# Performance work log

Hardware: AMD Instinct MI355X
Metric: run time of the kernel (lower is better)

The kernel has to match this reference:

```python
import jax, jax.numpy as jnp
import numpy as np

INPUT_DIM = 512
N_TREES = 64
TREE_DEPTH = 3
N_LEAVES = 2 ** TREE_DEPTH      # 8
N_INTERNAL = 2 ** TREE_DEPTH - 1  # 7
PPT = N_INTERNAL * (INPUT_DIM + 1) + N_LEAVES * 2  # params per tree = 3607
BATCH = 65536


def setup_inputs() -> dict:
    key = jax.random.key(0)
    k1, k2, k3 = jax.random.split(key, 3)
    x = jax.random.normal(k1, (BATCH, INPUT_DIM), dtype=jnp.float32)
    tree_params = jax.random.normal(k2, (1, N_TREES * PPT), dtype=jnp.float32)
    tree_weights = jax.random.normal(k3, (1, N_TREES), dtype=jnp.float32)
    return {"x": x, "tree_params": tree_params, "tree_weights": tree_weights}


def reference(x, tree_params, tree_weights):
    # Unpack all trees at once: [T, ppt]
    p = tree_params[0].reshape(N_TREES, PPT)
    split_w = p[:, : N_INTERNAL * INPUT_DIM].reshape(N_TREES, N_INTERNAL, INPUT_DIM)
    split_b = p[:, N_INTERNAL * INPUT_DIM : N_INTERNAL * (INPUT_DIM + 1)]  # [T, I]
    leaf_logits = p[:, N_INTERNAL * (INPUT_DIM + 1) :].reshape(N_TREES, N_LEAVES, 2)

    # decisions: [B, T, I]
    decisions = jax.nn.sigmoid(jnp.einsum('bd,tid->bti', x, split_w) + split_b[None])

    # Replicate the original indexing quirk: leaf_probs column j (a tree NODE index)
    # gets factor d_i if j == 2i+1 (and j < n_leaves), (1-d_i) if j == 2i+2.
    # Column 0 remains 1.0; each other column gets exactly one factor.
    cols = []
    for j in range(N_LEAVES):
        if j == 0:
            cols.append(jnp.ones_like(decisions[:, :, 0]))
        elif j % 2 == 1:
            i = (j - 1) // 2
            cols.append(decisions[:, :, i] if i < N_INTERNAL else jnp.ones_like(decisions[:, :, 0]))
        else:
            i = (j - 2) // 2
            cols.append(1.0 - decisions[:, :, i] if i < N_INTERNAL else jnp.ones_like(decisions[:, :, 0]))
    leaf_probs = jnp.stack(cols, axis=-1)  # [B, T, L]
    leaf_probs = leaf_probs / (leaf_probs.sum(axis=-1, keepdims=True) + 1e-8)

    leaf_dist = jax.nn.softmax(leaf_logits, axis=-1)  # [T, L, 2]
    tree_out = jnp.einsum('btl,tlc->btc', leaf_probs, leaf_dist)  # [B, T, 2]
    return jnp.einsum('btc,t->bc', tree_out, tree_weights[0])  # [B, 2]
```

## Files before the change

kernel.cpp:

```cpp
#include <hip/hip_runtime.h>
#include <stdint.h>


#define KDIM 512
#define PPT 3607

typedef _Float16 f16x8 __attribute__((ext_vector_type(8)));
typedef float f32x4 __attribute__((ext_vector_type(4)));


__global__ __launch_bounds__(128) void prep_kernel(const float* __restrict__ p,
                                                   const float* __restrict__ tw,
                                                   _Float16* __restrict__ Wh,
                                                   float* __restrict__ biasN,
                                                   float* __restrict__ AB) {
    const int c = blockIdx.x;
    const int t = c >> 2, i = c & 3;
    const float* wsrc = p + t * PPT + i * KDIM;
    for (int k = threadIdx.x; k < KDIM; k += 128)
        Wh[c * KDIM + k] = (_Float16)wsrc[k];
    if (threadIdx.x == 0)
        biasN[c] = p[t * PPT + 7 * KDIM + i];
    if (threadIdx.x == 64 && c < 64) {
        const int tt = c;
        const float* lg = p + tt * PPT + 7 * 513;
        const float w = tw[tt];
        float ld[8][2];
#pragma unroll
        for (int j = 0; j < 8; ++j) {
            float a = lg[2 * j], b = lg[2 * j + 1];
            float m = fmaxf(a, b);
            float e0 = expf(a - m), e1 = expf(b - m);
            float s = e0 + e1;
            ld[j][0] = e0 / s; ld[j][1] = e1 / s;
        }
        float* o = AB + tt * 10;
#pragma unroll
        for (int cc = 0; cc < 2; ++cc) {
            o[0 + cc] = w * (ld[0][cc] + ld[2][cc] + ld[4][cc] + ld[6][cc]);
            o[2 + cc] = w * (ld[1][cc] - ld[2][cc]);
            o[4 + cc] = w * (ld[3][cc] - ld[4][cc]);
            o[6 + cc] = w * (ld[5][cc] - ld[6][cc]);
            o[8 + cc] = w * (ld[7][cc]);
        }
    }
}

#define XBUF_STRIDE 8192
#define W_BASE 16384
#define WBUF_STRIDE 16384
#define EPI_STRIDE 260
#define AB_OFF 66560
#define PART_OFF 69120
#define LDS_BYTES 73216

__device__ __forceinline__ void gll16(const void* g, void* l) {
    __builtin_amdgcn_global_load_lds((const __attribute__((address_space(1))) uint32_t*)g,
                                     (__attribute__((address_space(3))) uint32_t*)l, 16, 0, 0);
}

__device__ __forceinline__ f16x8 cvt8(float4 a, float4 b) {
    f16x8 h;
    h[0] = (_Float16)a.x; h[1] = (_Float16)a.y; h[2] = (_Float16)a.z; h[3] = (_Float16)a.w;
    h[4] = (_Float16)b.x; h[5] = (_Float16)b.y; h[6] = (_Float16)b.z; h[7] = (_Float16)b.w;
    return h;
}

__global__ __launch_bounds__(512, 4) void main_kernel(const float* __restrict__ X,
                                                      const _Float16* __restrict__ Wh,
                                                      const float* __restrict__ biasN,
                                                      const float* __restrict__ ABg,
                                                      float* __restrict__ out) {
    extern __shared__ char smem[];
    const int tid = threadIdx.x;
    const int lane = tid & 63;
    const int w = tid >> 6;
    const int wm = w >> 2;
    const int wn = w & 3;
    const int gr0 = blockIdx.x * 128;

    {
        float* abl = (float*)(smem + AB_OFF);
        for (int i = tid; i < 640; i += 512) abl[i] = ABg[i];
    }
    asm volatile("s_waitcnt vmcnt(0)" ::: "memory");

    const float* Xrow = X + (size_t)(gr0 + (tid >> 2)) * KDIM + (tid & 3) * 8;
    const int wOffX = ((tid >> 2) << 6) + ((((tid & 3) ^ ((tid >> 3) & 3))) << 4);

    const _Float16* srcW[2];
    int dW[2];
#pragma unroll
    for (int i = 0; i < 2; ++i) {
        int colW = i * 128 + w * 16 + (lane >> 2);
        int kW = ((lane & 3) << 3) ^ (((colW >> 1) & 3) << 3);
        srcW[i] = Wh + (size_t)colW * KDIM + kW;
        dW[i] = (i * 512 + w * 64 + lane) * 16;
    }

    const int kb = (lane >> 4) << 3;
    const int kws = kb ^ (((lane >> 1) & 3) << 3);
    const int bColBase = (wn * 64 + (lane & 15)) * 32;
    const int aOff = ((lane & 15) << 6)
                   + (((lane >> 4) ^ (((lane & 15) >> 1) & 3)) << 4);

    f32x4 acc[4][4];
#pragma unroll
    for (int rt = 0; rt < 4; ++rt)
#pragma unroll
        for (int nt = 0; nt < 4; ++nt)
            acc[rt][nt] = (f32x4){0.f, 0.f, 0.f, 0.f};

    float4 xr[2][2];

    {
        float4 x0a = *(const float4*)(Xrow + 0);
        float4 x0b = *(const float4*)(Xrow + 4);
        gll16(srcW[0] + 0 * 32, smem + W_BASE + 0 * WBUF_STRIDE + dW[0]);
        gll16(srcW[1] + 0 * 32, smem + W_BASE + 0 * WBUF_STRIDE + dW[1]);
        xr[1][0] = *(const float4*)(Xrow + 1 * 32);
        xr[1][1] = *(const float4*)(Xrow + 1 * 32 + 4);
        gll16(srcW[0] + 1 * 32, smem + W_BASE + 1 * WBUF_STRIDE + dW[0]);
        gll16(srcW[1] + 1 * 32, smem + W_BASE + 1 * WBUF_STRIDE + dW[1]);
        *(f16x8*)(smem + 0 * XBUF_STRIDE + wOffX) = cvt8(x0a, x0b);
    }

#pragma unroll 16
    for (int kt = 0; kt < 16; ++kt) {
        if (kt <= 13) {
            xr[kt & 1][0] = *(const float4*)(Xrow + (kt + 2) * 32);
            xr[kt & 1][1] = *(const float4*)(Xrow + (kt + 2) * 32 + 4);
        }
        if (kt <= 13)      asm volatile("s_waitcnt vmcnt(4)" ::: "memory");
        else if (kt == 14) asm volatile("s_waitcnt vmcnt(2)" ::: "memory");
        else               asm volatile("s_waitcnt vmcnt(0)" ::: "memory");
        __builtin_amdgcn_s_barrier();
        if (kt <= 13) {
            char* wb = smem + W_BASE + ((kt + 2) % 3) * WBUF_STRIDE;
            gll16(srcW[0] + (kt + 2) * 32, wb + dW[0]);
            gll16(srcW[1] + (kt + 2) * 32, wb + dW[1]);
        }
        if (kt <= 14)
            *(f16x8*)(smem + ((kt + 1) & 1) * XBUF_STRIDE + wOffX) =
                cvt8(xr[(kt + 1) & 1][0], xr[(kt + 1) & 1][1]);
        {
            const _Float16* Wl = (const _Float16*)(smem + W_BASE + (kt % 3) * WBUF_STRIDE);
            const char* Xl = smem + (kt & 1) * XBUF_STRIDE + wm * 4096;
            f16x8 bfr[4];
#pragma unroll
            for (int nt = 0; nt < 4; ++nt)
                bfr[nt] = *(const f16x8*)&Wl[bColBase + nt * 512 + kws];
#pragma unroll
            for (int rt = 0; rt < 4; ++rt) {
                f16x8 af = *(const f16x8*)(Xl + rt * 1024 + aOff);
#pragma unroll
                for (int nt = 0; nt < 4; ++nt)
                    acc[rt][nt] = __builtin_amdgcn_mfma_f32_16x16x32_f16(af, bfr[nt], acc[rt][nt], 0, 0, 0);
            }
        }
    }

    __syncthreads();

    for (int p = 0; p < 2; ++p) {
        if (wm == p) {
            float bl[4];
#pragma unroll
            for (int nt = 0; nt < 4; ++nt) bl[nt] = biasN[wn * 64 + nt * 16 + (lane & 15)];
            float* ep = (float*)smem;
#pragma unroll
            for (int rt = 0; rt < 4; ++rt)
#pragma unroll
                for (int nt = 0; nt < 4; ++nt) {
                    const int col = wn * 64 + nt * 16 + (lane & 15);
#pragma unroll
                    for (int reg = 0; reg < 4; ++reg) {
                        const int rowl = rt * 16 + ((lane >> 4) << 2) + reg;
                        float z = acc[rt][nt][reg] + bl[nt];
                        ep[rowl * EPI_STRIDE + col] = __builtin_amdgcn_rcpf(1.f + __expf(-z));
                    }
                }
        }
        __syncthreads();
        {
            const float* ep = (const float*)smem;
            const float* abl = (const float*)(smem + AB_OFF);
            float* pb = (float*)(smem + PART_OFF);
            const int r = lane;
            float s0 = 0.f, s1 = 0.f;
#pragma unroll
            for (int j = 0; j < 8; ++j) {
                const int t = w * 8 + j;
                float4 dv = *(const float4*)&ep[r * EPI_STRIDE + t * 4];
                const float* abt = &abl[t * 10];
                float inv = __builtin_amdgcn_rcpf(4.f + dv.w + 1e-8f);
                s0 += (abt[0] + dv.x * abt[2] + dv.y * abt[4] + dv.z * abt[6] + dv.w * abt[8]) * inv;
                s1 += (abt[1] + dv.x * abt[3] + dv.y * abt[5] + dv.z * abt[7] + dv.w * abt[9]) * inv;
            }
            pb[(w * 64 + r) * 2 + 0] = s0;
            pb[(w * 64 + r) * 2 + 1] = s1;
        }
        __syncthreads();
        if (tid < 128) {
            const float* pb = (const float*)(smem + PART_OFF);
            const int r = tid >> 1, c = tid & 1;
            float s = 0.f;
#pragma unroll
            for (int g = 0; g < 8; ++g) s += pb[(g * 64 + r) * 2 + c];
            out[(size_t)(gr0 + p * 64 + r) * 2 + c] = s;
        }
        if (p == 0) __syncthreads();
    }
}

extern "C" void kernel_launch(void* const* d_in, const int* in_sizes, int n_in,
                              void* d_out, int out_size, void* d_ws, size_t ws_size,
                              hipStream_t stream) {
    const float* x  = (const float*)d_in[0];
    const float* tp = (const float*)d_in[1];
    const float* tw = (const float*)d_in[2];
    float* out = (float*)d_out;

    _Float16* Wh = (_Float16*)d_ws;
    float* biasN = (float*)((char*)d_ws + 262144);
    float* AB    = (float*)((char*)d_ws + 263168);

    (void)hipFuncSetAttribute((const void*)reinterpret_cast<const void*>(&main_kernel),
                              hipFuncAttributeMaxDynamicSharedMemorySize, LDS_BYTES);

    prep_kernel<<<256, 128, 0, stream>>>(tp, tw, Wh, biasN, AB);
    main_kernel<<<512, 512, LDS_BYTES, stream>>>(x, Wh, biasN, AB, out);
}
```

Baseline: 42.37 us.

## Switch W staging to double buffering with nontemporal X loads

The main GEMM loop now keeps two LDS buffers for the f16 weight tiles instead of three. Weights are prefetched one k-step ahead rather than two, and each iteration is restructured into barrier, issue loads and store the converted X, wait on vmcnt and lgkmcnt, barrier, then compute. The X row loads become nontemporal loads to avoid polluting cache with streamed activations, and the X/A LDS swizzle is reformulated to a different, consistent XOR pattern. In exchange, each iteration carries a second barrier plus a full LDS wait, and the shorter weight prefetch distance gives less latency hiding.

```diff
diff --git a/kernel.cpp b/kernel.cpp
--- a/kernel.cpp
+++ b/kernel.cpp
@@ -46,12 +46,12 @@
     }
 }
 
-#define XBUF_STRIDE 8192
-#define W_BASE 16384
-#define WBUF_STRIDE 16384
-#define EPI_STRIDE 260
+#define XB_STRIDE 8192
+#define WB_BASE 16384
+#define WB_STRIDE 16384
+#define EPI_S 260
 #define AB_OFF 66560
-#define PART_OFF 69120
+#define P_OFF 69120
 #define LDS_BYTES 73216
 
 __device__ __forceinline__ void gll16(const void* g, void* l) {
@@ -59,7 +59,7 @@
                                      (__attribute__((address_space(3))) uint32_t*)l, 16, 0, 0);
 }
 
-__device__ __forceinline__ f16x8 cvt8(float4 a, float4 b) {
+__device__ __forceinline__ f16x8 cvt8(f32x4 a, f32x4 b) {
     f16x8 h;
     h[0] = (_Float16)a.x; h[1] = (_Float16)a.y; h[2] = (_Float16)a.z; h[3] = (_Float16)a.w;
     h[4] = (_Float16)b.x; h[5] = (_Float16)b.y; h[6] = (_Float16)b.z; h[7] = (_Float16)b.w;
@@ -77,6 +77,8 @@
     const int w = tid >> 6;
     const int wm = w >> 2;
     const int wn = w & 3;
+    const int r15 = lane & 15;
+    const int hi = lane >> 4;
     const int gr0 = blockIdx.x * 128;
 
     {
@@ -85,8 +87,9 @@
     }
     asm volatile("s_waitcnt vmcnt(0)" ::: "memory");
 
-    const float* Xrow = X + (size_t)(gr0 + (tid >> 2)) * KDIM + (tid & 3) * 8;
-    const int wOffX = ((tid >> 2) << 6) + ((((tid & 3) ^ ((tid >> 3) & 3))) << 4);
+    const int xrow = tid >> 2, xg = tid & 3;
+    const float* Xp = X + (size_t)(gr0 + xrow) * KDIM + xg * 8;
+    const int xw = xrow * 64 + ((xg ^ (xrow & 3)) << 4);
 
     const _Float16* srcW[2];
     int dW[2];
@@ -100,9 +103,8 @@
 
     const int kb = (lane >> 4) << 3;
     const int kws = kb ^ (((lane >> 1) & 3) << 3);
-    const int bColBase = (wn * 64 + (lane & 15)) * 32;
-    const int aOff = ((lane & 15) << 6)
-                   + (((lane >> 4) ^ (((lane & 15) >> 1) & 3)) << 4);
+    const int bColBase = (wn * 64 + r15) * 32;
+    const int aoff = (wm * 64 + r15) * 64 + ((hi ^ (r15 & 3)) << 4);
 
     f32x4 acc[4][4];
 #pragma unroll
@@ -111,48 +113,48 @@
         for (int nt = 0; nt < 4; ++nt)
             acc[rt][nt] = (f32x4){0.f, 0.f, 0.f, 0.f};
 
-    float4 xr[2][2];
+    f32x4 xr[2][2];
 
     {
-        float4 x0a = *(const float4*)(Xrow + 0);
-        float4 x0b = *(const float4*)(Xrow + 4);
-        gll16(srcW[0] + 0 * 32, smem + W_BASE + 0 * WBUF_STRIDE + dW[0]);
-        gll16(srcW[1] + 0 * 32, smem + W_BASE + 0 * WBUF_STRIDE + dW[1]);
-        xr[1][0] = *(const float4*)(Xrow + 1 * 32);
-        xr[1][1] = *(const float4*)(Xrow + 1 * 32 + 4);
-        gll16(srcW[0] + 1 * 32, smem + W_BASE + 1 * WBUF_STRIDE + dW[0]);
-        gll16(srcW[1] + 1 * 32, smem + W_BASE + 1 * WBUF_STRIDE + dW[1]);
-        *(f16x8*)(smem + 0 * XBUF_STRIDE + wOffX) = cvt8(x0a, x0b);
-    }
-
-#pragma unroll 16
+        xr[0][0] = __builtin_nontemporal_load((const f32x4*)(Xp));
+        xr[0][1] = __builtin_nontemporal_load((const f32x4*)(Xp + 4));
+        gll16(srcW[0], smem + WB_BASE + dW[0]);
+        gll16(srcW[1], smem + WB_BASE + dW[1]);
+        xr[1][0] = __builtin_nontemporal_load((const f32x4*)(Xp + 32));
+        xr[1][1] = __builtin_nontemporal_load((const f32x4*)(Xp + 32 + 4));
+        *(f16x8*)(smem + xw) = cvt8(xr[0][0], xr[0][1]);
+    }
+
+#pragma unroll
     for (int kt = 0; kt < 16; ++kt) {
         if (kt <= 13) {
-            xr[kt & 1][0] = *(const float4*)(Xrow + (kt + 2) * 32);
-            xr[kt & 1][1] = *(const float4*)(Xrow + (kt + 2) * 32 + 4);
-        }
+            xr[kt & 1][0] = __builtin_nontemporal_load((const f32x4*)(Xp + (size_t)(kt + 2) * 32));
+            xr[kt & 1][1] = __builtin_nontemporal_load((const f32x4*)(Xp + (size_t)(kt + 2) * 32 + 4));
+        }
+        __builtin_amdgcn_s_barrier();
+        if (kt <= 14) {
+            char* wb = smem + WB_BASE + ((kt + 1) & 1) * WB_STRIDE;
+            gll16(srcW[0] + (size_t)(kt + 1) * 32, wb + dW[0]);
+            gll16(srcW[1] + (size_t)(kt + 1) * 32, wb + dW[1]);
+        }
+        if (kt <= 14)
+            *(f16x8*)(smem + ((kt + 1) & 1) * XB_STRIDE + xw) =
+                cvt8(xr[(kt + 1) & 1][0], xr[(kt + 1) & 1][1]);
         if (kt <= 13)      asm volatile("s_waitcnt vmcnt(4)" ::: "memory");
         else if (kt == 14) asm volatile("s_waitcnt vmcnt(2)" ::: "memory");
         else               asm volatile("s_waitcnt vmcnt(0)" ::: "memory");
+        asm volatile("s_waitcnt lgkmcnt(0)" ::: "memory");
         __builtin_amdgcn_s_barrier();
-        if (kt <= 13) {
-            char* wb = smem + W_BASE + ((kt + 2) % 3) * WBUF_STRIDE;
-            gll16(srcW[0] + (kt + 2) * 32, wb + dW[0]);
-            gll16(srcW[1] + (kt + 2) * 32, wb + dW[1]);
-        }
-        if (kt <= 14)
-            *(f16x8*)(smem + ((kt + 1) & 1) * XBUF_STRIDE + wOffX) =
-                cvt8(xr[(kt + 1) & 1][0], xr[(kt + 1) & 1][1]);
         {
-            const _Float16* Wl = (const _Float16*)(smem + W_BASE + (kt % 3) * WBUF_STRIDE);
-            const char* Xl = smem + (kt & 1) * XBUF_STRIDE + wm * 4096;
+            const char* xb = smem + (kt & 1) * XB_STRIDE;
+            const _Float16* Wl = (const _Float16*)(smem + WB_BASE + (kt & 1) * WB_STRIDE);
             f16x8 bfr[4];
 #pragma unroll
             for (int nt = 0; nt < 4; ++nt)
                 bfr[nt] = *(const f16x8*)&Wl[bColBase + nt * 512 + kws];
 #pragma unroll
             for (int rt = 0; rt < 4; ++rt) {
-                f16x8 af = *(const f16x8*)(Xl + rt * 1024 + aOff);
+                f16x8 af = *(const f16x8*)(xb + aoff + rt * 1024);
 #pragma unroll
                 for (int nt = 0; nt < 4; ++nt)
                     acc[rt][nt] = __builtin_amdgcn_mfma_f32_16x16x32_f16(af, bfr[nt], acc[rt][nt], 0, 0, 0);
@@ -166,18 +168,18 @@
         if (wm == p) {
             float bl[4];
 #pragma unroll
-            for (int nt = 0; nt < 4; ++nt) bl[nt] = biasN[wn * 64 + nt * 16 + (lane & 15)];
+            for (int nt = 0; nt < 4; ++nt) bl[nt] = biasN[wn * 64 + nt * 16 + r15];
             float* ep = (float*)smem;
 #pragma unroll
             for (int rt = 0; rt < 4; ++rt)
 #pragma unroll
                 for (int nt = 0; nt < 4; ++nt) {
-                    const int col = wn * 64 + nt * 16 + (lane & 15);
+                    const int col = wn * 64 + nt * 16 + r15;
 #pragma unroll
                     for (int reg = 0; reg < 4; ++reg) {
-                        const int rowl = rt * 16 + ((lane >> 4) << 2) + reg;
+                        const int rowl = rt * 16 + hi * 4 + reg;
                         float z = acc[rt][nt][reg] + bl[nt];
-                        ep[rowl * EPI_STRIDE + col] = __builtin_amdgcn_rcpf(1.f + __expf(-z));
+                        ep[rowl * EPI_S + col] = __builtin_amdgcn_rcpf(1.f + __expf(-z));
                     }
                 }
         }
@@ -185,13 +187,13 @@
         {
             const float* ep = (const float*)smem;
             const float* abl = (const float*)(smem + AB_OFF);
-            float* pb = (float*)(smem + PART_OFF);
+            float* pb = (float*)(smem + P_OFF);
             const int r = lane;
             float s0 = 0.f, s1 = 0.f;
 #pragma unroll
             for (int j = 0; j < 8; ++j) {
                 const int t = w * 8 + j;
-                float4 dv = *(const float4*)&ep[r * EPI_STRIDE + t * 4];
+                float4 dv = *(const float4*)&ep[r * EPI_S + t * 4];
                 const float* abt = &abl[t * 10];
                 float inv = __builtin_amdgcn_rcpf(4.f + dv.w + 1e-8f);
                 s0 += (abt[0] + dv.x * abt[2] + dv.y * abt[4] + dv.z * abt[6] + dv.w * abt[8]) * inv;
@@ -202,7 +204,7 @@
         }
         __syncthreads();
         if (tid < 128) {
-            const float* pb = (const float*)(smem + PART_OFF);
+            const float* pb = (const float*)(smem + P_OFF);
             const int r = tid >> 1, c = tid & 1;
             float s = 0.f;
 #pragma unroll
```

New measurement: 51.00 us. 1.2x slower.
